# Performance work log

Hardware: AMD Instinct MI355X
Metric: run time of the kernel (lower is better)

Reference implementation:

```python
import jax, jax.numpy as jnp
import numpy as np

UNITS = 512
GROUPS = 32
EPS = 1e-3  # keras GroupNormalization default epsilon


def group_norm(x, gamma, beta):
    # x: [B,H,W,C]; normalize over (H,W, channels-within-group)
    B, H, W, C = x.shape
    xg = x.reshape(B, H, W, GROUPS, C // GROUPS)
    mean = xg.mean(axis=(1, 2, 4), keepdims=True)
    var = xg.var(axis=(1, 2, 4), keepdims=True)
    xn = (xg - mean) * jax.lax.rsqrt(var + EPS)
    return xn.reshape(B, H, W, C) * gamma + beta


def setup_inputs() -> dict:
    key = jax.random.key(0)
    ks = jax.random.split(key, 6)
    B, H, W, C = 16, 32, 32, UNITS
    std = 0.02  # RandomNormal(stddev=0.02) kernel init
    return {
        "x": jax.random.normal(ks[0], (B, H, W, C), jnp.float32),
        "gamma": jnp.ones((C,), jnp.float32),
        "beta": jnp.zeros((C,), jnp.float32),
        "Wq": std * jax.random.normal(ks[1], (C, UNITS), jnp.float32),
        "bq": jnp.zeros((UNITS,), jnp.float32),
        "Wk": std * jax.random.normal(ks[2], (C, UNITS), jnp.float32),
        "bk": jnp.zeros((UNITS,), jnp.float32),
        "Wv": std * jax.random.normal(ks[3], (C, UNITS), jnp.float32),
        "bv": jnp.zeros((UNITS,), jnp.float32),
        "Wp": std * jax.random.normal(ks[4], (UNITS, UNITS), jnp.float32),
        "bp": jnp.zeros((UNITS,), jnp.float32),
    }


def reference(x, gamma, beta, Wq, bq, Wk, bk, Wv, bv, Wp, bp):
    B, H, W, C = x.shape
    scale = jnp.float32(UNITS) ** -0.5
    xn = group_norm(x, gamma, beta)  # note: original residual uses normalized input
    # flatten spatial dims to N = H*W tokens (same math as bhwc/bHWc einsums)
    xf = xn.reshape(B, H * W, C)
    q = xf @ Wq + bq
    k = xf @ Wk + bk
    v = xf @ Wv + bv
    scores = jnp.einsum('bnc,bmc->bnm', q, k) * scale  # [B, N, N]
    attn = jax.nn.softmax(scores, axis=-1)
    out = jnp.einsum('bnm,bmc->bnc', attn, v)
    proj = out @ Wp + bp
    return xn + proj.reshape(B, H, W, C)
```

## Files before the change

### kernel.cpp

```cpp
#include <hip/hip_runtime.h>
#include <math.h>

#define BATCH 16
#define NTOK  1024
#define CH    512
#define NGRP  32
#define GSZ   16
#define EPSV  1e-3f
#define MTOT  (BATCH*NTOK)
#define SCALE 0.04419417382415922f
#define SEXP  (SCALE*1.4426950408889634f)

typedef unsigned short u16;
typedef __attribute__((ext_vector_type(4))) float f32x4;
typedef __attribute__((ext_vector_type(8))) short s16x8;

__device__ __forceinline__ u16 f2bf(float f) {
    union { float f; unsigned u; } x{f};
    unsigned r = x.u + 0x7fff + ((x.u >> 16) & 1);
    return (u16)(r >> 16);
}

__device__ __forceinline__ void gld16(const u16* g, u16* l) {
    __builtin_amdgcn_global_load_lds(
        (const __attribute__((address_space(1))) void*)g,
        (__attribute__((address_space(3))) void*)l, 16, 0, 0);
}

__global__ __launch_bounds__(256) void gn_stats(const float* __restrict__ x,
                                                float2* __restrict__ stats) {
    int bg = blockIdx.x;
    int b = bg >> 5, g = bg & 31;
    const float* base = x + (size_t)b * NTOK * CH + g * GSZ;
    float s = 0.f, ss = 0.f;
    for (int i = threadIdx.x; i < 4096; i += 256) {
        int p = i >> 2, c4 = i & 3;
        float4 v = *(const float4*)(base + (size_t)p * CH + c4 * 4);
        s  += v.x + v.y + v.z + v.w;
        ss += v.x * v.x + v.y * v.y + v.z * v.z + v.w * v.w;
    }
    for (int off = 32; off; off >>= 1) {
        s  += __shfl_down(s, off);
        ss += __shfl_down(ss, off);
    }
    __shared__ float2 part[4];
    if ((threadIdx.x & 63) == 0) part[threadIdx.x >> 6] = make_float2(s, ss);
    __syncthreads();
    if (threadIdx.x == 0) {
        float S = 0.f, SS = 0.f;
        for (int i = 0; i < 4; i++) { S += part[i].x; SS += part[i].y; }
        float mean = S * (1.f / 16384.f);
        float var  = SS * (1.f / 16384.f) - mean * mean;
        stats[bg] = make_float2(mean, rsqrtf(var + EPSV));
    }
}

__global__ __launch_bounds__(256) void gn_apply(const float* __restrict__ x,
                                                const float2* __restrict__ stats,
                                                const float* __restrict__ gamma,
                                                const float* __restrict__ beta,
                                                float* __restrict__ xn,
                                                u16* __restrict__ xnb) {
    size_t total = (size_t)MTOT * CH / 4;
    for (size_t i4 = (size_t)blockIdx.x * 256 + threadIdx.x; i4 < total;
         i4 += (size_t)gridDim.x * 256) {
        size_t flat = i4 * 4;
        int c = (int)(flat & (CH - 1));
        int b = (int)(flat >> 19);
        int g = c >> 4;
        float2 st = stats[(b << 5) + g];
        float4 xv = *(const float4*)(x + flat);
        float4 gv = *(const float4*)(gamma + c);
        float4 bv = *(const float4*)(beta + c);
        float4 o;
        o.x = (xv.x - st.x) * st.y * gv.x + bv.x;
        o.y = (xv.y - st.x) * st.y * gv.y + bv.y;
        o.z = (xv.z - st.x) * st.y * gv.z + bv.z;
        o.w = (xv.w - st.x) * st.y * gv.w + bv.w;
        *(float4*)(xn + flat) = o;
        uint2 h;
        h.x = (unsigned)f2bf(o.x) | ((unsigned)f2bf(o.y) << 16);
        h.y = (unsigned)f2bf(o.z) | ((unsigned)f2bf(o.w) << 16);
        *(uint2*)(xnb + flat) = h;
    }
}

__global__ __launch_bounds__(256) void weights_prep(
    const float* __restrict__ Wq, const float* __restrict__ Wk,
    const float* __restrict__ Wv, const float* __restrict__ Wp,
    u16* __restrict__ WTqkv, u16* __restrict__ WTp) {
    int z = blockIdx.z;
    const float* src = z == 0 ? Wq : z == 1 ? Wk : z == 2 ? Wv : Wp;
    u16* dst = z < 3 ? WTqkv + (size_t)z * CH * CH : WTp;
    __shared__ u16 tile[64][66];
    int r0 = blockIdx.y * 64, c0 = blockIdx.x * 64;
    int t = threadIdx.x;
    for (int i = 0; i < 16; i++) {
        int idx = i * 256 + t;
        int r = idx >> 6, c = idx & 63;
        tile[r][c] = f2bf(src[(size_t)(r0 + r) * CH + c0 + c]);
    }
    __syncthreads();
    for (int i = 0; i < 16; i++) {
        int idx = i * 256 + t;
        int oc = idx >> 6, orr = idx & 63;
        dst[(size_t)(c0 + oc) * CH + r0 + orr] = tile[orr][oc];
    }
}

__global__ void prep_bias(const float* __restrict__ bq, const float* __restrict__ bk,
                          const float* __restrict__ bv, float* __restrict__ bqkv) {
    int t = blockIdx.x * 256 + threadIdx.x;
    bqkv[t] = t < 512 ? bq[t] : (t < 1024 ? bk[t - 512] : bv[t - 1024]);
}

__global__ __launch_bounds__(256) void vt_transpose(const u16* __restrict__ in,
                                                    u16* __restrict__ out,
                                                    int R, int C, int ldIn,
                                                    long sIn, long sOut) {
    __shared__ u16 tile[64][66];
    int z = blockIdx.z;
    in  += (size_t)z * sIn;
    out += (size_t)z * sOut;
    int r0 = blockIdx.y * 64, c0 = blockIdx.x * 64;
    int t = threadIdx.x;
    for (int i = 0; i < 16; i++) {
        int idx = i * 256 + t;
        int r = idx >> 6, c = idx & 63;
        tile[r][c] = in[(size_t)(r0 + r) * ldIn + c0 + c];
    }
    __syncthreads();
    for (int i = 0; i < 16; i++) {
        int idx = i * 256 + t;
        int oc = idx >> 6, orr = idx & 63;
        out[(size_t)(c0 + oc) * R + r0 + orr] = tile[orr][oc];
    }
}

template <bool BIAS, bool RES, bool OUTF32>
__global__ __launch_bounds__(256) void gemm_bt(
    const u16* __restrict__ A, const u16* __restrict__ B, void* __restrict__ Cout,
    const float* __restrict__ bias, const float* __restrict__ res,
    int K, int lda, int ldb, int ldc,
    long sA, long sB, long sC, float alpha) {
    __shared__ __align__(16) u16 Asm[4096];
    __shared__ __align__(16) u16 Bsm[4096];

    unsigned flat = blockIdx.x + gridDim.x * (blockIdx.y + gridDim.y * blockIdx.z);
    unsigned nb = gridDim.x * gridDim.y * gridDim.z;
    unsigned lf = (flat & 7) * (nb >> 3) + (flat >> 3);
    unsigned pb = gridDim.x * gridDim.y;
    unsigned bz = lf / pb, rem = lf - bz * pb;
    unsigned by = rem / gridDim.x, bx = rem - by * gridDim.x;

    A += (size_t)bz * sA;
    B += (size_t)bz * sB;
    size_t zc = (size_t)bz * sC;

    int t = threadIdx.x;
    int wave = t >> 6, lane = t & 63;
    int wm = wave >> 1, wn = wave & 1;
    int rowA0 = by * 128;
    int colB0 = bx * 128;

    int c16log = (lane & 3) ^ ((lane >> 3) & 3);
    const u16* aG[2]; const u16* bG[2]; u16* aL[2]; u16* bL[2];
#pragma unroll
    for (int j = 0; j < 2; j++) {
        int s = wave * 2 + j;
        int row = s * 16 + (lane >> 2);
        aL[j] = Asm + s * 512;
        bL[j] = Bsm + s * 512;
        aG[j] = A + (size_t)(rowA0 + row) * lda + c16log * 8;
        bG[j] = B + (size_t)(colB0 + row) * ldb + c16log * 8;
    }

    int kg = lane >> 4;
    int aoff[4], boff[4];
#pragma unroll
    for (int i = 0; i < 4; i++) {
        int ra = wm * 64 + i * 16 + (lane & 15);
        aoff[i] = ra * 32 + (kg ^ ((ra >> 1) & 3)) * 8;
        int rb = wn * 64 + i * 16 + (lane & 15);
        boff[i] = rb * 32 + (kg ^ ((rb >> 1) & 3)) * 8;
    }

    f32x4 acc[4][4] = {};
    for (int kt = 0; kt < K; kt += 32) {
        gld16(aG[0] + kt, aL[0]);
        gld16(aG[1] + kt, aL[1]);
        gld16(bG[0] + kt, bL[0]);
        gld16(bG[1] + kt, bL[1]);
        __syncthreads();
        s16x8 af[4], bfr[4];
#pragma unroll
        for (int i = 0; i < 4; i++) {
            af[i]  = *(const s16x8*)(Asm + aoff[i]);
            bfr[i] = *(const s16x8*)(Bsm + boff[i]);
        }
#pragma unroll
        for (int mi = 0; mi < 4; mi++)
#pragma unroll
            for (int nj = 0; nj < 4; nj++)
                acc[mi][nj] = __builtin_amdgcn_mfma_f32_16x16x32_bf16(
                    af[mi], bfr[nj], acc[mi][nj], 0, 0, 0);
        __syncthreads();
    }

    int r0 = rowA0 + wm * 64 + (lane >> 4) * 4;
    int c0c = colB0 + wn * 64 + (lane & 15);
#pragma unroll
    for (int mi = 0; mi < 4; mi++) {
#pragma unroll
        for (int nj = 0; nj < 4; nj++) {
            int c = c0c + nj * 16;
            float bv = BIAS ? bias[c] : 0.f;
            f32x4 v = acc[mi][nj];
#pragma unroll
            for (int j = 0; j < 4; j++) {
                int rr = r0 + mi * 16 + j;
                float val = v[j] * alpha + bv;
                if (RES) val += res[(size_t)rr * ldc + c];
                if (OUTF32) ((float*)Cout)[zc + (size_t)rr * ldc + c] = val;
                else        ((u16*)Cout)[zc + (size_t)rr * ldc + c] = f2bf(val);
            }
        }
    }
}

__global__ __launch_bounds__(512, 2) void attn_fused(const u16* __restrict__ qkv,
                                                     u16* __restrict__ P) {
    __shared__ __align__(16) u16 Bsm[32768];

    unsigned flat = blockIdx.x;
    unsigned lf = (flat & 7) * 32 + (flat >> 3);
    int b = lf >> 4, mt = lf & 15;

    int t = threadIdx.x, w = t >> 6, lane = t & 63;
    int wr = w >> 1, wn = w & 1;
    int l15 = lane & 15, kg = lane >> 4;

    const u16* qbase = qkv + ((size_t)b * NTOK + mt * 64) * (3 * CH);
    const u16* kbase = qkv + (size_t)b * NTOK * (3 * CH) + CH;

    const u16* qrow = qbase + (size_t)(wr * 16 + l15) * (3 * CH) + kg * 8;
    s16x8 aq[16];
#pragma unroll
    for (int kt = 0; kt < 16; kt++) aq[kt] = *(const s16x8*)(qrow + kt * 32);

    int c16log = (lane & 3) ^ ((lane >> 3) & 3);
    const u16* bG[8];
#pragma unroll
    for (int j = 0; j < 8; j++) {
        int row = (w * 8 + j) * 16 + (lane >> 2);
        bG[j] = kbase + (size_t)row * (3 * CH) + c16log * 8;
    }
    int rb0 = wn * 512 + l15;
    int boff = rb0 * 32 + (kg ^ ((rb0 >> 1) & 3)) * 8;

    f32x4 acc[32];
#pragma unroll
    for (int i = 0; i < 32; i++) acc[i] = f32x4{0.f, 0.f, 0.f, 0.f};

#pragma unroll
    for (int kt = 0; kt < 16; kt++) {
#pragma unroll
        for (int j = 0; j < 8; j++)
            gld16(bG[j] + kt * 32, Bsm + (w * 8 + j) * 512);
        __syncthreads();
#pragma unroll
        for (int nj = 0; nj < 32; nj++) {
            s16x8 bf = *(const s16x8*)(Bsm + boff + nj * 512);
            acc[nj] = __builtin_amdgcn_mfma_f32_16x16x32_bf16(aq[kt], bf, acc[nj], 0, 0, 0);
        }
        __syncthreads();
    }

    float* redm = (float*)Bsm;
    float* reds = (float*)(Bsm + 256);

    float mrow[4], inv[4], srow[4];
#pragma unroll
    for (int j = 0; j < 4; j++) {
        float m = acc[0][j];
#pragma unroll
        for (int nj = 1; nj < 32; nj++) m = fmaxf(m, acc[nj][j]);
        for (int off = 1; off < 16; off <<= 1) m = fmaxf(m, __shfl_xor(m, off));
        mrow[j] = m;
    }
    if (l15 == 0) {
#pragma unroll
        for (int j = 0; j < 4; j++) redm[(wr * 16 + kg * 4 + j) * 2 + wn] = mrow[j];
    }
    __syncthreads();
#pragma unroll
    for (int j = 0; j < 4; j++) {
        int row = wr * 16 + kg * 4 + j;
        mrow[j] = fmaxf(redm[row * 2], redm[row * 2 + 1]);
    }
#pragma unroll
    for (int j = 0; j < 4; j++) {
        float s = 0.f;
#pragma unroll
        for (int nj = 0; nj < 32; nj++) {
            float e = exp2f((acc[nj][j] - mrow[j]) * SEXP);
            acc[nj][j] = e;
            s += e;
        }
        for (int off = 1; off < 16; off <<= 1) s += __shfl_xor(s, off);
        srow[j] = s;
    }
    if (l15 == 0) {
#pragma unroll
        for (int j = 0; j < 4; j++) reds[(wr * 16 + kg * 4 + j) * 2 + wn] = srow[j];
    }
    __syncthreads();
#pragma unroll
    for (int j = 0; j < 4; j++) {
        int row = wr * 16 + kg * 4 + j;
        inv[j] = 1.f / (reds[row * 2] + reds[row * 2 + 1]);
    }

    size_t pbase = (size_t)b * NTOK * NTOK + (size_t)mt * 64 * NTOK;
#pragma unroll
    for (int h = 0; h < 2; h++) {
        __syncthreads();
        if (wn == h) {
#pragma unroll
            for (int nj = 0; nj < 32; nj++) {
                int c = nj * 16 + l15;
                int c16 = c >> 3, cw = c & 7;
#pragma unroll
                for (int j = 0; j < 4; j++) {
                    int row = wr * 16 + kg * 4 + j;
                    int pc16 = c16 ^ ((row >> 2) & 7);
                    Bsm[row * 512 + pc16 * 8 + cw] = f2bf(acc[nj][j] * inv[j]);
                }
            }
        }
        __syncthreads();
#pragma unroll
        for (int i = 0; i < 8; i++) {
            int flat16 = (i * 512 + t) * 8;
            int row = flat16 >> 9, c = flat16 & 511;
            int pc16 = (c >> 3) ^ ((row >> 2) & 7);
            uint4 vv = *(const uint4*)(Bsm + row * 512 + pc16 * 8);
            *(uint4*)(P + pbase + (size_t)row * NTOK + h * 512 + c) = vv;
        }
    }
}

extern "C" void kernel_launch(void* const* d_in, const int* in_sizes, int n_in,
                              void* d_out, int out_size, void* d_ws, size_t ws_size,
                              hipStream_t stream) {
    const float* x     = (const float*)d_in[0];
    const float* gamma = (const float*)d_in[1];
    const float* beta  = (const float*)d_in[2];
    const float* Wq    = (const float*)d_in[3];
    const float* bq    = (const float*)d_in[4];
    const float* Wk    = (const float*)d_in[5];
    const float* bk    = (const float*)d_in[6];
    const float* Wv    = (const float*)d_in[7];
    const float* bv    = (const float*)d_in[8];
    const float* Wp    = (const float*)d_in[9];
    const float* bp    = (const float*)d_in[10];
    float* out = (float*)d_out;

    const size_t SZ  = (size_t)MTOT * CH;
    const size_t NSZ = (size_t)NTOK * CH;
    const size_t SCB = (size_t)NTOK * NTOK;

    char* p = (char*)d_ws;
    float*  xn    = (float*)p;   p += SZ * 4;
    u16*    xnb   = (u16*)p;     p += SZ * 2;
    u16*    qkvb  = (u16*)p;     p += (size_t)MTOT * 3 * CH * 2;
    u16*    vt    = (u16*)p;     p += SZ * 2;
    u16*    ao    = (u16*)p;     p += SZ * 2;
    u16*    P     = (u16*)p;     p += (size_t)BATCH * SCB * 2;
    u16*    WTqkv = (u16*)p;     p += (size_t)3 * CH * CH * 2;
    u16*    WTp   = (u16*)p;     p += (size_t)CH * CH * 2;
    float*  bqkv  = (float*)p;   p += 3 * CH * 4;
    float2* stats = (float2*)p;

    dim3 blk(256);

    gn_stats<<<BATCH * NGRP, blk, 0, stream>>>(x, stats);
    gn_apply<<<2048, blk, 0, stream>>>(x, stats, gamma, beta, xn, xnb);
    weights_prep<<<dim3(8, 8, 4), blk, 0, stream>>>(Wq, Wk, Wv, Wp, WTqkv, WTp);
    prep_bias<<<6, blk, 0, stream>>>(bq, bk, bv, bqkv);

    gemm_bt<true, false, false><<<dim3(12, 128, 1), blk, 0, stream>>>(
        xnb, WTqkv, qkvb, bqkv, nullptr, CH, CH, CH, 3 * CH, 0, 0, 0, 1.f);

    vt_transpose<<<dim3(8, 16, BATCH), blk, 0, stream>>>(
        qkvb + 2 * CH, vt, NTOK, CH, 3 * CH, (long)NTOK * 3 * CH, (long)NSZ);

    attn_fused<<<256, 512, 0, stream>>>(qkvb, P);

    gemm_bt<false, false, false><<<dim3(4, 8, BATCH), blk, 0, stream>>>(
        P, vt, ao, nullptr, nullptr, NTOK, NTOK, NTOK, CH,
        (long)SCB, (long)NSZ, (long)NSZ, 1.f);

    gemm_bt<true, true, true><<<dim3(4, 128, 1), blk, 0, stream>>>(
        ao, WTp, out, bp, xn, CH, CH, CH, CH, 0, 0, 0, 1.f);
}
```

Before: 270.0 us.

## Double-buffer LDS staging in GEMM and attention score loops

Both the bf16 GEMM main loop and the attention QK^T loop now keep two LDS buffers. The next K-slice is issued with global_load_lds while MFMAs consume the current one, and one barrier per iteration is dropped. The aim is to hide global-load latency behind compute. In exchange, LDS per block doubles: 32KB for the GEMM and 128KB for attn_fused. That likely stops two attention blocks fitting per CU despite launch_bounds(512,2).

```diff
diff --git a/kernel.cpp b/kernel.cpp
--- a/kernel.cpp
+++ b/kernel.cpp
@@ -143,8 +143,8 @@
     const float* __restrict__ bias, const float* __restrict__ res,
     int K, int lda, int ldb, int ldc,
     long sA, long sB, long sC, float alpha) {
-    __shared__ __align__(16) u16 Asm[4096];
-    __shared__ __align__(16) u16 Bsm[4096];
+    __shared__ __align__(16) u16 Asm[8192];
+    __shared__ __align__(16) u16 Bsm[8192];
 
     unsigned flat = blockIdx.x + gridDim.x * (blockIdx.y + gridDim.y * blockIdx.z);
     unsigned nb = gridDim.x * gridDim.y * gridDim.z;
@@ -185,18 +185,27 @@
         boff[i] = rb * 32 + (kg ^ ((rb >> 1) & 3)) * 8;
     }
 
+#define STG_G(buf, ktE)                          \
+    {                                            \
+        gld16(aG[0] + (ktE), aL[0] + (buf) * 4096); \
+        gld16(aG[1] + (ktE), aL[1] + (buf) * 4096); \
+        gld16(bG[0] + (ktE), bL[0] + (buf) * 4096); \
+        gld16(bG[1] + (ktE), bL[1] + (buf) * 4096); \
+    }
+
     f32x4 acc[4][4] = {};
-    for (int kt = 0; kt < K; kt += 32) {
-        gld16(aG[0] + kt, aL[0]);
-        gld16(aG[1] + kt, aL[1]);
-        gld16(bG[0] + kt, bL[0]);
-        gld16(bG[1] + kt, bL[1]);
-        __syncthreads();
+    int nk = K >> 5;
+    STG_G(0, 0);
+    __syncthreads();
+    for (int kt = 0; kt < nk; kt++) {
+        if (kt + 1 < nk) STG_G((kt + 1) & 1, (kt + 1) * 32);
+        const u16* as = Asm + (kt & 1) * 4096;
+        const u16* bs = Bsm + (kt & 1) * 4096;
         s16x8 af[4], bfr[4];
 #pragma unroll
         for (int i = 0; i < 4; i++) {
-            af[i]  = *(const s16x8*)(Asm + aoff[i]);
-            bfr[i] = *(const s16x8*)(Bsm + boff[i]);
+            af[i]  = *(const s16x8*)(as + aoff[i]);
+            bfr[i] = *(const s16x8*)(bs + boff[i]);
         }
 #pragma unroll
         for (int mi = 0; mi < 4; mi++)
@@ -206,6 +215,7 @@
                     af[mi], bfr[nj], acc[mi][nj], 0, 0, 0);
         __syncthreads();
     }
+#undef STG_G
 
     int r0 = rowA0 + wm * 64 + (lane >> 4) * 4;
     int c0c = colB0 + wn * 64 + (lane & 15);
@@ -230,7 +240,7 @@
 
 __global__ __launch_bounds__(512, 2) void attn_fused(const u16* __restrict__ qkv,
                                                      u16* __restrict__ P) {
-    __shared__ __align__(16) u16 Bsm[32768];
+    __shared__ __align__(16) u16 Bsm[65536];
 
     unsigned flat = blockIdx.x;
     unsigned lf = (flat & 7) * 32 + (flat >> 3);
@@ -262,19 +272,27 @@
 #pragma unroll
     for (int i = 0; i < 32; i++) acc[i] = f32x4{0.f, 0.f, 0.f, 0.f};
 
+#define STG(buf, kt)                                                        \
+    {                                                                       \
+        _Pragma("unroll")                                                   \
+        for (int j = 0; j < 8; j++)                                         \
+            gld16(bG[j] + (kt) * 32, Bsm + (buf) * 32768 + (w * 8 + j) * 512); \
+    }
+
+    STG(0, 0);
+    __syncthreads();
 #pragma unroll
     for (int kt = 0; kt < 16; kt++) {
-#pragma unroll
-        for (int j = 0; j < 8; j++)
-            gld16(bG[j] + kt * 32, Bsm + (w * 8 + j) * 512);
+        if (kt < 15) STG((kt + 1) & 1, kt + 1);
+        const u16* bb = Bsm + (kt & 1) * 32768;
+#pragma unroll
+        for (int nj = 0; nj < 32; nj++) {
+            s16x8 bf = *(const s16x8*)(bb + boff + nj * 512);
+            acc[nj] = __builtin_amdgcn_mfma_f32_16x16x32_bf16(aq[kt], bf, acc[nj], 0, 0, 0);
+        }
         __syncthreads();
-#pragma unroll
-        for (int nj = 0; nj < 32; nj++) {
-            s16x8 bf = *(const s16x8*)(Bsm + boff + nj * 512);
-            acc[nj] = __builtin_amdgcn_mfma_f32_16x16x32_bf16(aq[kt], bf, acc[nj], 0, 0, 0);
-        }
-        __syncthreads();
-    }
+    }
+#undef STG
 
     float* redm = (float*)Bsm;
     float* reds = (float*)(Bsm + 256);
```

New measurement: 262.2 us. -2.9%, faster.
